# Optimization experiments

Measured on AMD Instinct MI355X. Metric: run time of the kernel, lower is better.

The kernel has to match this reference:

```python
import jax, jax.numpy as jnp
from jax import lax
import numpy as np

B, L, E, K, NCLS = 128, 1024, 8, 3, 5


def conv1d(x, w, b):
    # x: [N,C,L], w: [O,I,3], padding=1 -> same length
    y = lax.conv_general_dilated(x, w, (1,), [(1, 1)], dimension_numbers=('NCH', 'OIH', 'NCH'))
    return y + b[None, :, None]


def maxpool2(x):
    # MaxPool1d(kernel=2, stride=2), floor mode (VALID drops odd tail)
    return lax.reduce_window(x, -jnp.inf, lax.max, (1, 1, 2), (1, 1, 2), 'VALID')


def setup_inputs():
    key = jax.random.key(0)
    ks = jax.random.split(key, 32)
    s = 0.05
    g = lambda i, shp: jax.random.normal(ks[i], shp, jnp.float32) * s
    inp = {}
    inp['x'] = jax.random.normal(ks[0], (B, 1, L), jnp.float32)
    inp['c1_w'], inp['c1_b'] = g(1, (16, 1, 3)), jnp.zeros((16,), jnp.float32)
    # stacked expert conv params (leading dim = E)
    chans = [(16, 16), (16, 32), (32, 64), (64, 128), (128, 256), (256, 512)]
    for j, (ci, co) in enumerate(chans, start=1):
        inp[f'ew{j}'] = g(1 + j, (E, co, ci, 3))
        inp[f'eb{j}'] = jnp.zeros((E, co), jnp.float32)
    inp['r_w'], inp['r_b'] = g(10, (E, 16)), jnp.zeros((E,), jnp.float32)
    inp['c2_w'], inp['c2_b'] = g(11, (1024, 512, 3)), jnp.zeros((1024,), jnp.float32)
    fl = (L // 8 // 2) * 1024
    inp['f1_w'], inp['f1_b'] = g(12, (256, fl)) * 0.2, jnp.zeros((256,), jnp.float32)
    inp['f2_w'], inp['f2_b'] = g(13, (NCLS, 256)), jnp.zeros((NCLS,), jnp.float32)
    return inp


def reference(x, c1_w, c1_b, ew1, eb1, ew2, eb2, ew3, eb3, ew4, eb4, ew5, eb5, ew6, eb6,
              r_w, r_b, c2_w, c2_b, f1_w, f1_b, f2_w, f2_b):
    b = x.shape[0]
    h = jax.nn.relu(conv1d(x, c1_w, c1_b))            # [B,16,L]
    pooled = h.mean(axis=-1)                           # AdaptiveAvgPool1d(1) -> [B,16]
    # (router noise skipped: eval-mode determinism)
    rlogits = pooled @ r_w.T + r_b                     # [B,E]
    probs = jax.nn.softmax(rlogits, axis=-1)
    tg, ti = lax.top_k(probs, K)                       # [B,K]
    tg = tg / tg.sum(axis=-1, keepdims=True)
    gates = jnp.zeros((b, E), probs.dtype).at[jnp.arange(b)[:, None], ti].set(tg)  # dense [B,E]

    def expert(w1, b1, w2, b2, w3, b3, w4, b4, w5, b5, w6, b6):
        y = conv1d(h, w1, b1)
        y = maxpool2(jax.nn.relu(conv1d(y, w2, b2)))   # block1 -> [B,32,L/2]
        y = conv1d(y, w3, b3)
        y = maxpool2(jax.nn.relu(conv1d(y, w4, b4)))   # block2 -> [B,128,L/4]
        y = conv1d(y, w5, b5)
        y = maxpool2(jax.nn.relu(conv1d(y, w6, b6)))   # block3 -> [B,512,L/8]
        return y

    eouts = jax.vmap(expert)(ew1, eb1, ew2, eb2, ew3, eb3, ew4, eb4, ew5, eb5, ew6, eb6)  # [E,B,512,L/8]
    combined = jnp.einsum('be,ebcl->bcl', gates, eouts)  # gated scatter-combine (zero gate == not dispatched)

    y = maxpool2(jax.nn.relu(conv1d(combined, c2_w, c2_b)))  # [B,1024,L/16]
    y = y.reshape(b, -1)
    y = jax.nn.relu(y @ f1_w.T + f1_b)                 # dropout p=0.05 is identity in eval
    out = y @ f2_w.T + f2_b                            # [B,NCLS]

    mean_probs = probs.mean(axis=0)
    cv = jnp.std(mean_probs, ddof=1) / (mean_probs.mean() + 1e-10)  # torch std is unbiased
    return out, cv ** 2
```

## Files before the change

### kernel.cpp

```cpp
#include <hip/hip_runtime.h>
#include <hip/hip_bf16.h>
#include <math.h>

#define B_   128
#define L_   1024
#define E_   8
#define K_   3

typedef float f32x4 __attribute__((ext_vector_type(4)));
typedef short s8v  __attribute__((ext_vector_type(8)));
typedef unsigned short u16x8 __attribute__((ext_vector_type(8)));

__device__ inline ushort f2bf(float v) {
  union { float f; unsigned u; } x; x.f = v;
  unsigned r = (x.u + 0x7fffu + ((x.u >> 16) & 1u)) >> 16;
  return (ushort)r;
}
__device__ inline float bf2f(ushort h) {
  union { unsigned u; float f; } x; x.u = ((unsigned)h) << 16;
  return x.f;
}

__device__ __forceinline__ void gload_lds16(const ushort* g, ushort* l) {
  __builtin_amdgcn_global_load_lds(
      (const __attribute__((address_space(1))) unsigned int*)g,
      (__attribute__((address_space(3))) unsigned int*)l, 16, 0, 0);
}

__global__ __launch_bounds__(256) void conv1_k(
    const float* __restrict__ x, const float* __restrict__ w,
    const float* __restrict__ bias, float* __restrict__ h,
    float* __restrict__ pooled)
{
  const int b = blockIdx.x;
  const int t = threadIdx.x;
  __shared__ float xs[1026];
  __shared__ float wsm[48];
  __shared__ float bs[16];
  __shared__ float red[4][16];

  for (int i = t; i < 1024; i += 256) xs[i + 1] = x[(size_t)b * 1024 + i];
  if (t == 0) { xs[0] = 0.f; xs[1025] = 0.f; }
  if (t < 48) wsm[t] = w[t];
  if (t < 16) bs[t] = bias[t];
  __syncthreads();

  float ps[16];
#pragma unroll
  for (int c = 0; c < 16; ++c) ps[c] = 0.f;

  for (int li = 0; li < 4; ++li) {
    const int l = t + li * 256;
    const float xm = xs[l], x0 = xs[l + 1], xp = xs[l + 2];
#pragma unroll
    for (int co = 0; co < 16; ++co) {
      float v = fmaf(wsm[co * 3 + 0], xm,
                fmaf(wsm[co * 3 + 1], x0,
                fmaf(wsm[co * 3 + 2], xp, bs[co])));
      v = fmaxf(v, 0.f);
      h[((size_t)b * 16 + co) * 1024 + l] = v;
      ps[co] += v;
    }
  }
#pragma unroll
  for (int co = 0; co < 16; ++co) {
    float v = ps[co];
    for (int off = 32; off > 0; off >>= 1) v += __shfl_down(v, off, 64);
    ps[co] = v;
  }
  const int wid = t >> 6, lane = t & 63;
  if (lane == 0) {
#pragma unroll
    for (int co = 0; co < 16; ++co) red[wid][co] = ps[co];
  }
  __syncthreads();
  if (t < 16) pooled[(size_t)b * 16 + t] =
      (red[0][t] + red[1][t] + red[2][t] + red[3][t]) * (1.f / 1024.f);
}

__global__ void router_k(const float* __restrict__ pooled,
                         const float* __restrict__ rw,
                         const float* __restrict__ rb,
                         float* __restrict__ pair_g, int* __restrict__ pair_e,
                         float* __restrict__ cv2_out)
{
  const int b = threadIdx.x;
  __shared__ float pl[128][8];
  __shared__ float mp[8];

  float pv[16];
#pragma unroll
  for (int i = 0; i < 16; ++i) pv[i] = pooled[(size_t)b * 16 + i];

  float lg[8];
#pragma unroll
  for (int e = 0; e < 8; ++e) {
    float s = rb[e];
#pragma unroll
    for (int i = 0; i < 16; ++i) s = fmaf(pv[i], rw[e * 16 + i], s);
    lg[e] = s;
  }
  float mx = lg[0];
#pragma unroll
  for (int e = 1; e < 8; ++e) mx = fmaxf(mx, lg[e]);
  float pr[8]; float sum = 0.f;
#pragma unroll
  for (int e = 0; e < 8; ++e) { pr[e] = expf(lg[e] - mx); sum += pr[e]; }
  const float inv = 1.f / sum;
#pragma unroll
  for (int e = 0; e < 8; ++e) { pr[e] *= inv; pl[b][e] = pr[e]; }

  bool used[8] = {false,false,false,false,false,false,false,false};
  float tg[3]; int ti[3];
  for (int k = 0; k < 3; ++k) {
    float best = -1.f; int bi = 0;
#pragma unroll
    for (int e = 0; e < 8; ++e)
      if (!used[e] && pr[e] > best) { best = pr[e]; bi = e; }
    used[bi] = true; tg[k] = best; ti[k] = bi;
  }
  const float ts = 1.f / (tg[0] + tg[1] + tg[2]);
  for (int k = 0; k < 3; ++k) {
    pair_g[b * 3 + k] = tg[k] * ts;
    pair_e[b * 3 + k] = ti[k];
  }
  __syncthreads();
  if (b < 8) {
    float s = 0.f;
    for (int i = 0; i < 128; ++i) s += pl[i][b];
    mp[b] = s * (1.f / 128.f);
  }
  __syncthreads();
  if (b == 0) {
    float m = 0.f;
    for (int e = 0; e < 8; ++e) m += mp[e];
    m *= (1.f / 8.f);
    float v = 0.f;
    for (int e = 0; e < 8; ++e) { float d = mp[e] - m; v += d * d; }
    v *= (1.f / 7.f);
    const float cv = sqrtf(v) / (m + 1e-10f);
    cv2_out[0] = cv * cv;
  }
}

template <int CI, int CO, int LIN, bool POOL, int CIC, int CO_T, int CO_R,
          int IN_DIV>
__global__ __launch_bounds__(256) void convR_k(
    const float* __restrict__ in, const float* __restrict__ w,
    const float* __restrict__ bias, float* __restrict__ out,
    const int* __restrict__ pe)
{
  constexpr int CQ  = CO_T / CO_R;
  constexpr int LQ  = 256 / CQ;
  constexpr int L_T = LQ * 4;
  constexpr int LOUT = POOL ? (LIN / 2) : LIN;
  constexpr int RS  = L_T + 8;
  constexpr int CG  = CO_R / 4;

  const int p  = blockIdx.x;
  const int cb = blockIdx.y * CO_T;
  const int l0 = blockIdx.z * L_T;
  const int e  = pe ? pe[p] : 0;
  const float* inp = in + (size_t)(p / IN_DIV) * CI * LIN;
  const float* wp  = w + (size_t)e * CO * CI * 3;

  __shared__ float in_s[CIC * RS];
  __shared__ float w_s[CIC * 3 * CO_T];

  const int t  = threadIdx.x;
  const int cq = t / LQ;
  const int lq = t % LQ;

  float acc[CO_R][4];
#pragma unroll
  for (int c = 0; c < CO_R; ++c)
#pragma unroll
    for (int l = 0; l < 4; ++l) acc[c][l] = 0.f;

  for (int c0 = 0; c0 < CI; c0 += CIC) {
    for (int idx = t; idx < CIC * (L_T + 2); idx += 256) {
      const int ci = idx / (L_T + 2);
      const int j  = idx - ci * (L_T + 2);
      const int gl = l0 + j - 1;
      in_s[ci * RS + j] =
          (gl >= 0 && gl < LIN) ? inp[(size_t)(c0 + ci) * LIN + gl] : 0.f;
    }
    for (int i = t; i < CIC * CO_T; i += 256) {
      const int co = i % CO_T;
      const int ci = i / CO_T;
      const float* wsrc = wp + ((size_t)(cb + co) * CI + (c0 + ci)) * 3;
      const float w0 = wsrc[0], w1 = wsrc[1], w2 = wsrc[2];
      w_s[(ci * 3 + 0) * CO_T + co] = w0;
      w_s[(ci * 3 + 1) * CO_T + co] = w1;
      w_s[(ci * 3 + 2) * CO_T + co] = w2;
    }
    __syncthreads();
#pragma unroll 4
    for (int ci = 0; ci < CIC; ++ci) {
      const float* row = &in_s[ci * RS + lq * 4];
      const float4 xa = *reinterpret_cast<const float4*>(row);
      const float2 xb = *reinterpret_cast<const float2*>(row + 4);
      const float xv[6] = {xa.x, xa.y, xa.z, xa.w, xb.x, xb.y};
      const float* wrow = &w_s[ci * 3 * CO_T + cq * CO_R];
#pragma unroll
      for (int k = 0; k < 3; ++k) {
#pragma unroll
        for (int cg = 0; cg < CG; ++cg) {
          const float4 wv =
              *reinterpret_cast<const float4*>(&wrow[k * CO_T + cg * 4]);
          const float wq[4] = {wv.x, wv.y, wv.z, wv.w};
#pragma unroll
          for (int c = 0; c < 4; ++c)
#pragma unroll
            for (int l = 0; l < 4; ++l)
              acc[cg * 4 + c][l] = fmaf(wq[c], xv[l + k], acc[cg * 4 + c][l]);
        }
      }
    }
    __syncthreads();
  }

#pragma unroll
  for (int c = 0; c < CO_R; ++c) {
    const int co = cb + cq * CO_R + c;
    const float bv = bias[(size_t)e * CO + co];
    const float v0 = acc[c][0] + bv, v1 = acc[c][1] + bv;
    const float v2 = acc[c][2] + bv, v3 = acc[c][3] + bv;
    float* op = out + ((size_t)p * CO + co) * LOUT;
    if (POOL) {
      const int lo = (l0 >> 1) + lq * 2;
      float2 r;
      r.x = fmaxf(fmaxf(v0, v1), 0.f);
      r.y = fmaxf(fmaxf(v2, v3), 0.f);
      *reinterpret_cast<float2*>(&op[lo]) = r;
    } else {
      const int l = l0 + lq * 4;
      *reinterpret_cast<float4*>(&op[l]) = make_float4(v0, v1, v2, v3);
    }
  }
}

__global__ void wprep_k(const float* __restrict__ w, ushort* __restrict__ oh,
                        ushort* __restrict__ ol, int E, int CO, int CI,
                        int total)
{
  const int idx = blockIdx.x * 256 + threadIdx.x;
  if (idx >= total) return;
  const int KC = CI >> 5;
  const int j = idx & 31;
  int r = idx >> 5;
  const int co = r % CO; r /= CO;
  const int kc = r % KC; r /= KC;
  const int tp = r % 3;
  const int e  = r / 3;
  const float v = w[(((size_t)e * CO + co) * CI + (kc * 32 + j)) * 3 + tp];
  const ushort hi = f2bf(v);
  oh[idx] = hi;
  ol[idx] = f2bf(v - bf2f(hi));
}

__global__ __launch_bounds__(256) void t0_k(const float* __restrict__ in,
                                            ushort* __restrict__ oh,
                                            ushort* __restrict__ ol)
{
  __shared__ float tile[32][33];
  const int p  = blockIdx.x;
  const int l0 = blockIdx.y * 32;
  const int tx = threadIdx.x & 31;
  const int ty = threadIdx.x >> 5;

#pragma unroll
  for (int i = 0; i < 4; ++i) {
    const int ci = ty + i * 8;
    tile[ci][tx] = in[(size_t)p * 16384 + (size_t)ci * 512 + l0 + tx];
  }
  __syncthreads();
#pragma unroll
  for (int i = 0; i < 4; ++i) {
    const int l = l0 + ty + i * 8;
    const float v = tile[tx][ty + i * 8];
    const size_t o = ((size_t)p * 514 + 1 + l) * 32 + tx;
    const ushort hi = f2bf(v);
    oh[o] = hi;
    ol[o] = f2bf(v - bf2f(hi));
  }
  if (blockIdx.y == 0 && threadIdx.x < 32) {
    const size_t o0 = (size_t)p * 514 * 32 + threadIdx.x;
    const size_t o1 = ((size_t)p * 514 + 513) * 32 + threadIdx.x;
    oh[o0] = 0; ol[o0] = 0; oh[o1] = 0; ol[o1] = 0;
  }
}

__global__ __launch_bounds__(256) void t2_k(const float* __restrict__ comb,
                                            ushort* __restrict__ oh,
                                            ushort* __restrict__ ol)
{
  const size_t o4 = ((size_t)blockIdx.x * 256 + threadIdx.x) * 4;
  const int p = (int)(o4 / 66560);
  const int rem = (int)(o4 - (size_t)p * 66560);
  const int r = rem >> 9;
  const int c = rem & 511;
  ushort4 h4, l4;
  if (r == 0 || r == 129) {
    h4 = make_ushort4(0, 0, 0, 0);
    l4 = make_ushort4(0, 0, 0, 0);
  } else {
    const float4 v =
        *reinterpret_cast<const float4*>(&comb[((size_t)p * 128 + (r - 1)) * 512 + c]);
    h4.x = f2bf(v.x); l4.x = f2bf(v.x - bf2f(h4.x));
    h4.y = f2bf(v.y); l4.y = f2bf(v.y - bf2f(h4.y));
    h4.z = f2bf(v.z); l4.z = f2bf(v.z - bf2f(h4.z));
    h4.w = f2bf(v.w); l4.w = f2bf(v.w - bf2f(h4.w));
  }
  *reinterpret_cast<ushort4*>(&oh[o4]) = h4;
  *reinterpret_cast<ushort4*>(&ol[o4]) = l4;
}

template <int CI, int CO, int L, int OMODE>
__global__ __launch_bounds__(256) void convM_k(
    const ushort* __restrict__ xh, const ushort* __restrict__ xl,
    const ushort* __restrict__ wh, const ushort* __restrict__ wl,
    const float* __restrict__ bias,
    ushort* __restrict__ oh, ushort* __restrict__ ol,
    float* __restrict__ of,
    const int* __restrict__ pe, const float* __restrict__ pg,
    int pair0, int kpass)
{
  constexpr int KC = CI / 32;
  const int bx = blockIdx.x;
  const int cb = blockIdx.y * 64;
  const int lz = blockIdx.z * 128;

  int e = 0; float gate = 1.f;
  if (OMODE != 2) e = pe[pair0 + bx];
  if (OMODE == 1) gate = pg[pair0 + bx];
  const int lp = bx;

  __shared__ ushort xs[2][130][32];
  __shared__ ushort wsm[2][3][64][32];
  ushort* xsf = &xs[0][0][0];
  ushort* wsf = &wsm[0][0][0][0];

  const int t = threadIdx.x;
  const int lane = t & 63;
  const int wv = t >> 6;
  const int l16 = lane & 15;
  const int kb8 = (lane >> 4) * 8;

  f32x4 acc[2][4];
#pragma unroll
  for (int a = 0; a < 2; ++a)
#pragma unroll
    for (int b = 0; b < 4; ++b) acc[a][b] = (f32x4){0.f, 0.f, 0.f, 0.f};

  const size_t xbase = ((size_t)lp * (L + 2) + lz) * CI;

  for (int kc = 0; kc < KC; ++kc) {
    const int c0 = kc * 32;
#pragma unroll
    for (int it = 0; it < 5; ++it) {
      const int g = it * 256 + t;
      if (g < 1040) {
        const int pl = g >= 520;
        const int r = g - pl * 520;
        const int row = r >> 2;
        const int c16 = r & 3;
        const ushort* src =
            (pl ? xl : xh) + xbase + (size_t)row * CI + c0 + c16 * 8;
        gload_lds16(src, xsf + (size_t)g * 8);
      }
    }
#pragma unroll
    for (int it = 0; it < 6; ++it) {
      const int g = it * 256 + t;
      const int pl = g >= 768;
      const int r = g - pl * 768;
      const int tp = r >> 8;
      const int rr = r & 255;
      const int co = rr >> 2;
      const int c16 = rr & 3;
      const ushort* src = (pl ? wl : wh) +
          ((((size_t)e * 3 + tp) * KC + kc) * CO + cb + co) * 32 + c16 * 8;
      gload_lds16(src, wsf + (size_t)g * 8);
    }
    __syncthreads();

#pragma unroll
    for (int tp = 0; tp < 3; ++tp) {
      const int ar = wv * 32 + l16 + tp;
      s8v a00 = *reinterpret_cast<const s8v*>(&xs[0][ar][kb8]);
      s8v a01 = *reinterpret_cast<const s8v*>(&xs[0][ar + 16][kb8]);
      s8v a10 = *reinterpret_cast<const s8v*>(&xs[1][ar][kb8]);
      s8v a11 = *reinterpret_cast<const s8v*>(&xs[1][ar + 16][kb8]);
#pragma unroll
      for (int cs = 0; cs < 4; ++cs) {
        const int brow = cs * 16 + l16;
        s8v bh = *reinterpret_cast<const s8v*>(&wsm[0][tp][brow][kb8]);
        s8v bl = *reinterpret_cast<const s8v*>(&wsm[1][tp][brow][kb8]);
        acc[0][cs] = __builtin_amdgcn_mfma_f32_16x16x32_bf16(a00, bh, acc[0][cs], 0, 0, 0);
        acc[0][cs] = __builtin_amdgcn_mfma_f32_16x16x32_bf16(a00, bl, acc[0][cs], 0, 0, 0);
        acc[0][cs] = __builtin_amdgcn_mfma_f32_16x16x32_bf16(a10, bh, acc[0][cs], 0, 0, 0);
        acc[1][cs] = __builtin_amdgcn_mfma_f32_16x16x32_bf16(a01, bh, acc[1][cs], 0, 0, 0);
        acc[1][cs] = __builtin_amdgcn_mfma_f32_16x16x32_bf16(a01, bl, acc[1][cs], 0, 0, 0);
        acc[1][cs] = __builtin_amdgcn_mfma_f32_16x16x32_bf16(a11, bh, acc[1][cs], 0, 0, 0);
      }
    }
    __syncthreads();
  }

  float bv[4];
#pragma unroll
  for (int cs = 0; cs < 4; ++cs)
    bv[cs] = bias[(size_t)e * CO + cb + cs * 16 + l16];

  if (OMODE == 0) {
#pragma unroll
    for (int ls = 0; ls < 2; ++ls)
#pragma unroll
      for (int cs = 0; cs < 4; ++cs)
#pragma unroll
        for (int r = 0; r < 4; ++r) {
          const int l = lz + wv * 32 + ls * 16 + (lane >> 4) * 4 + r;
          const float v = acc[ls][cs][r] + bv[cs];
          const size_t o = ((size_t)lp * (L + 2) + 1 + l) * CO + cb + cs * 16 + l16;
          const ushort hi = f2bf(v);
          oh[o] = hi;
          ol[o] = f2bf(v - bf2f(hi));
        }
    if (blockIdx.z == 0 && t < 64) {
      const size_t o0 = (size_t)lp * (L + 2) * CO + cb + t;
      const size_t o1 = ((size_t)lp * (L + 2) + (L + 1)) * CO + cb + t;
      oh[o0] = 0; ol[o0] = 0; oh[o1] = 0; ol[o1] = 0;
    }
  } else if (OMODE == 3) {
#pragma unroll
    for (int ls = 0; ls < 2; ++ls)
#pragma unroll
      for (int cs = 0; cs < 4; ++cs)
#pragma unroll
        for (int r = 0; r < 4; r += 2) {
          const float v0 = acc[ls][cs][r] + bv[cs];
          const float v1 = acc[ls][cs][r + 1] + bv[cs];
          const float m = fmaxf(fmaxf(v0, v1), 0.f);
          const int lpp = (lz + wv * 32 + ls * 16 + (lane >> 4) * 4 + r) >> 1;
          const size_t o = ((size_t)lp * (L / 2 + 2) + 1 + lpp) * CO + cb + cs * 16 + l16;
          const ushort hi = f2bf(m);
          oh[o] = hi;
          ol[o] = f2bf(m - bf2f(hi));
        }
    if (blockIdx.z == 0 && t < 64) {
      const size_t o0 = (size_t)lp * (L / 2 + 2) * CO + cb + t;
      const size_t o1 = ((size_t)lp * (L / 2 + 2) + (L / 2 + 1)) * CO + cb + t;
      oh[o0] = 0; ol[o0] = 0; oh[o1] = 0; ol[o1] = 0;
    }
  } else if (OMODE == 1) {
#pragma unroll
    for (int ls = 0; ls < 2; ++ls)
#pragma unroll
      for (int cs = 0; cs < 4; ++cs)
#pragma unroll
        for (int r = 0; r < 4; r += 2) {
          const float v0 = acc[ls][cs][r] + bv[cs];
          const float v1 = acc[ls][cs][r + 1] + bv[cs];
          const float m = fmaxf(fmaxf(v0, v1), 0.f);
          const int lpp = (lz + wv * 32 + ls * 16 + (lane >> 4) * 4 + r) >> 1;
          const int co = cb + cs * 16 + l16;
          of[((size_t)bx * (L / 2) + lpp) * CO + co] = gate * m;
        }
  } else {
#pragma unroll
    for (int ls = 0; ls < 2; ++ls)
#pragma unroll
      for (int cs = 0; cs < 4; ++cs)
#pragma unroll
        for (int r = 0; r < 4; r += 2) {
          const float v0 = acc[ls][cs][r] + bv[cs];
          const float v1 = acc[ls][cs][r + 1] + bv[cs];
          const float m = fmaxf(fmaxf(v0, v1), 0.f);
          const int lpp = (lz + wv * 32 + ls * 16 + (lane >> 4) * 4 + r) >> 1;
          const int co = cb + cs * 16 + l16;
          const size_t o = ((size_t)lp * CO + co) * (L / 2) + lpp;
          of[o] = m;
        }
  }
}

__global__ void combine3_k(const float4* __restrict__ y6,
                           float4* __restrict__ outc, int total4)
{
  const int idx = blockIdx.x * 256 + threadIdx.x;
  if (idx >= total4) return;
  const int b = idx >> 14;
  const int r = idx & 16383;
  const float4 a = y6[(size_t)(b * 3 + 0) * 16384 + r];
  const float4 c = y6[(size_t)(b * 3 + 1) * 16384 + r];
  const float4 d = y6[(size_t)(b * 3 + 2) * 16384 + r];
  float4 o;
  o.x = a.x + c.x + d.x;
  o.y = a.y + c.y + d.y;
  o.z = a.z + c.z + d.z;
  o.w = a.w + c.w + d.w;
  outc[idx] = o;
}

__global__ __launch_bounds__(256) void fc1M_k(const float* __restrict__ X,
                                              const float* __restrict__ W,
                                              float* __restrict__ part)
{
  __shared__ ushort xs[2][128][32];
  __shared__ ushort wsm[2][64][32];
  const int t = threadIdx.x;
  const int lane = t & 63;
  const int wv = t >> 6;
  const int l16 = lane & 15;
  const int kb8 = (lane >> 4) * 8;
  const int ot = blockIdx.x * 64;
  const size_t k0g = (size_t)blockIdx.y * 512;

  f32x4 acc[2][4];
#pragma unroll
  for (int a = 0; a < 2; ++a)
#pragma unroll
    for (int b = 0; b < 4; ++b) acc[a][b] = (f32x4){0.f, 0.f, 0.f, 0.f};

  const int xrow = t >> 1;
  const int xcol = (t & 1) * 16;
  const int wco  = t >> 2;
  const int wk   = (t & 3) * 8;

  for (int it = 0; it < 16; ++it) {
    const size_t k0 = k0g + it * 32;
    {
      const float* src = X + (size_t)xrow * 65536 + k0 + xcol;
      float v[16];
#pragma unroll
      for (int q = 0; q < 4; ++q)
        *reinterpret_cast<float4*>(&v[q * 4]) =
            *reinterpret_cast<const float4*>(src + q * 4);
#pragma unroll
      for (int q = 0; q < 2; ++q) {
        u16x8 hv, lv;
#pragma unroll
        for (int j = 0; j < 8; ++j) {
          const float f = v[q * 8 + j];
          const ushort h = f2bf(f);
          hv[j] = h;
          lv[j] = f2bf(f - bf2f(h));
        }
        *reinterpret_cast<u16x8*>(&xs[0][xrow][xcol + q * 8]) = hv;
        *reinterpret_cast<u16x8*>(&xs[1][xrow][xcol + q * 8]) = lv;
      }
    }
    {
      const float* src = W + (size_t)(ot + wco) * 65536 + k0 + wk;
      float v[8];
      *reinterpret_cast<float4*>(&v[0]) = *reinterpret_cast<const float4*>(src);
      *reinterpret_cast<float4*>(&v[4]) = *reinterpret_cast<const float4*>(src + 4);
      u16x8 hv, lv;
#pragma unroll
      for (int j = 0; j < 8; ++j) {
        const ushort h = f2bf(v[j]);
        hv[j] = h;
        lv[j] = f2bf(v[j] - bf2f(h));
      }
      *reinterpret_cast<u16x8*>(&wsm[0][wco][wk]) = hv;
      *reinterpret_cast<u16x8*>(&wsm[1][wco][wk]) = lv;
    }
    __syncthreads();
#pragma unroll
    for (int ms = 0; ms < 2; ++ms) {
      const int ar = wv * 32 + ms * 16 + l16;
      s8v ah = *reinterpret_cast<const s8v*>(&xs[0][ar][kb8]);
      s8v al = *reinterpret_cast<const s8v*>(&xs[1][ar][kb8]);
#pragma unroll
      for (int cs = 0; cs < 4; ++cs) {
        const int brow = cs * 16 + l16;
        s8v bh = *reinterpret_cast<const s8v*>(&wsm[0][brow][kb8]);
        s8v bl = *reinterpret_cast<const s8v*>(&wsm[1][brow][kb8]);
        acc[ms][cs] = __builtin_amdgcn_mfma_f32_16x16x32_bf16(ah, bh, acc[ms][cs], 0, 0, 0);
        acc[ms][cs] = __builtin_amdgcn_mfma_f32_16x16x32_bf16(ah, bl, acc[ms][cs], 0, 0, 0);
        acc[ms][cs] = __builtin_amdgcn_mfma_f32_16x16x32_bf16(al, bh, acc[ms][cs], 0, 0, 0);
      }
    }
    __syncthreads();
  }

#pragma unroll
  for (int ms = 0; ms < 2; ++ms)
#pragma unroll
    for (int cs = 0; cs < 4; ++cs)
#pragma unroll
      for (int r = 0; r < 4; ++r) {
        const int row = wv * 32 + ms * 16 + (lane >> 4) * 4 + r;
        const int col = ot + cs * 16 + l16;
        part[((size_t)blockIdx.y * 128 + row) * 256 + col] = acc[ms][cs][r];
      }
}

__global__ void fc1red_k(const float* __restrict__ part,
                         const float* __restrict__ b1, float* __restrict__ o1)
{
  const int idx = blockIdx.x * 256 + threadIdx.x;
  if (idx < 32768) {
    float s = 0.f;
#pragma unroll 8
    for (int z = 0; z < 128; ++z) s += part[(size_t)z * 32768 + idx];
    o1[idx] = fmaxf(s + b1[idx & 255], 0.f);
  }
}

__global__ void fc2_k(const float* __restrict__ o1, const float* __restrict__ w2,
                      const float* __restrict__ b2, float* __restrict__ out)
{
  const int b = blockIdx.x;
  const int lane = threadIdx.x;
  float acc[5] = {0.f, 0.f, 0.f, 0.f, 0.f};
  for (int i = lane; i < 256; i += 64) {
    const float xv = o1[(size_t)b * 256 + i];
#pragma unroll
    for (int o = 0; o < 5; ++o) acc[o] = fmaf(xv, w2[o * 256 + i], acc[o]);
  }
#pragma unroll
  for (int o = 0; o < 5; ++o) {
    for (int off = 32; off > 0; off >>= 1)
      acc[o] += __shfl_down(acc[o], off, 64);
  }
  if (lane == 0) {
#pragma unroll
    for (int o = 0; o < 5; ++o) out[b * 5 + o] = acc[o] + b2[o];
  }
}

extern "C" void kernel_launch(void* const* d_in, const int* in_sizes, int n_in,
                              void* d_out, int out_size, void* d_ws,
                              size_t ws_size, hipStream_t stream)
{
  const float* x   = (const float*)d_in[0];
  const float* c1w = (const float*)d_in[1];
  const float* c1b = (const float*)d_in[2];
  const float* ew[6];
  const float* eb[6];
  for (int j = 0; j < 6; ++j) {
    ew[j] = (const float*)d_in[3 + 2 * j];
    eb[j] = (const float*)d_in[4 + 2 * j];
  }
  const float* rw  = (const float*)d_in[15];
  const float* rb  = (const float*)d_in[16];
  const float* c2w = (const float*)d_in[17];
  const float* c2b = (const float*)d_in[18];
  const float* f1w = (const float*)d_in[19];
  const float* f1b = (const float*)d_in[20];
  const float* f2w = (const float*)d_in[21];
  const float* f2b = (const float*)d_in[22];
  float* out = (float*)d_out;

  const int chunkB = (ws_size >= 170000000ull) ? 32 : 16;
  const int chunkP = chunkB * 3;
  const int nchunk = 128 / chunkB;

  char* basep = (char*)d_ws;
  size_t off = 0;
  auto alloc = [&](size_t bytes) -> void* {
    off = (off + 255) & ~(size_t)255;
    void* r = basep + off;
    off += bytes;
    return r;
  };

  float* h      = (float*)alloc(2097152ull * 4);
  float* pooled = (float*)alloc(2048ull * 4);
  float* pairg  = (float*)alloc(384ull * 4);
  int*   paire  = (int*)  alloc(384ull * 4);
  float* fc1o   = (float*)alloc(32768ull * 4);
  float* comb   = (float*)alloc(8388608ull * 4);
  const size_t chunk_base = (off + 255) & ~(size_t)255;
  float*  bufA  = (float*)alloc((size_t)chunkP * 16384 * 4);
  float*  bufB  = (float*)alloc((size_t)chunkP * 16384 * 4);
  ushort* xt3h  = (ushort*)alloc((size_t)chunkP * 16448 * 2);
  ushort* xt3l  = (ushort*)alloc((size_t)chunkP * 16448 * 2);
  ushort* yE3h  = (ushort*)alloc((size_t)chunkP * 32896 * 2);
  ushort* yE3l  = (ushort*)alloc((size_t)chunkP * 32896 * 2);
  ushort* xt5h  = (ushort*)alloc((size_t)chunkP * 33024 * 2);
  ushort* xt5l  = (ushort*)alloc((size_t)chunkP * 33024 * 2);
  ushort* y5h   = (ushort*)alloc((size_t)chunkP * 66048 * 2);
  ushort* y5l   = (ushort*)alloc((size_t)chunkP * 66048 * 2);
  float*  y6    = (float*)alloc((size_t)chunkP * 65536 * 4);
  ushort* xtFh  = (ushort*)(basep + chunk_base);
  ushort* xtFl  = xtFh + 8519680ull;
  float* part   = (float*)(basep + chunk_base);
  ushort* wp3h  = (ushort*)alloc(49152ull * 2);
  ushort* wp3l  = (ushort*)alloc(49152ull * 2);
  ushort* wp4h  = (ushort*)alloc(196608ull * 2);
  ushort* wp4l  = (ushort*)alloc(196608ull * 2);
  ushort* wp5h  = (ushort*)alloc(786432ull * 2);
  ushort* wp5l  = (ushort*)alloc(786432ull * 2);
  ushort* wp6h  = (ushort*)alloc(3145728ull * 2);
  ushort* wp6l  = (ushort*)alloc(3145728ull * 2);
  ushort* wpFh  = (ushort*)alloc(1572864ull * 2);
  ushort* wpFl  = (ushort*)alloc(1572864ull * 2);

  conv1_k<<<128, 256, 0, stream>>>(x, c1w, c1b, h, pooled);
  router_k<<<1, 128, 0, stream>>>(pooled, rw, rb, pairg, paire, out + 640);

  wprep_k<<<(49152 + 255) / 256, 256, 0, stream>>>(ew[2], wp3h, wp3l, 8, 64, 32, 49152);
  wprep_k<<<(196608 + 255) / 256, 256, 0, stream>>>(ew[3], wp4h, wp4l, 8, 128, 64, 196608);
  wprep_k<<<(786432 + 255) / 256, 256, 0, stream>>>(ew[4], wp5h, wp5l, 8, 256, 128, 786432);
  wprep_k<<<(3145728 + 255) / 256, 256, 0, stream>>>(ew[5], wp6h, wp6l, 8, 512, 256, 3145728);
  wprep_k<<<(1572864 + 255) / 256, 256, 0, stream>>>(c2w, wpFh, wpFl, 1, 1024, 512, 1572864);

  for (int c = 0; c < nchunk; ++c) {
    const int b0 = c * chunkB;
    const int p0 = c * chunkP;
    convR_k<16, 16, 1024, false, 16, 16, 4, 3>
        <<<dim3(chunkP, 1, 4), 256, 0, stream>>>(
            h + (size_t)b0 * 16 * 1024, ew[0], eb[0], bufA, paire + p0);
    convR_k<16, 32, 1024, true, 16, 32, 8, 1>
        <<<dim3(chunkP, 1, 4), 256, 0, stream>>>(bufA, ew[1], eb[1], bufB,
                                                 paire + p0);
    t0_k<<<dim3(chunkP, 16), 256, 0, stream>>>(bufB, xt3h, xt3l);
    convM_k<32, 64, 512, 0>
        <<<dim3(chunkP, 1, 4), 256, 0, stream>>>(xt3h, xt3l, wp3h, wp3l, eb[2],
                                                 yE3h, yE3l, nullptr, paire,
                                                 nullptr, p0, 0);
    convM_k<64, 128, 512, 3>
        <<<dim3(chunkP, 2, 4), 256, 0, stream>>>(yE3h, yE3l, wp4h, wp4l, eb[3],
                                                 xt5h, xt5l, nullptr, paire,
                                                 nullptr, p0, 0);
    convM_k<128, 256, 256, 0>
        <<<dim3(chunkP, 4, 2), 256, 0, stream>>>(xt5h, xt5l, wp5h, wp5l, eb[4],
                                                 y5h, y5l, nullptr, paire,
                                                 nullptr, p0, 0);
    convM_k<256, 512, 256, 1>
        <<<dim3(chunkP, 8, 2), 256, 0, stream>>>(y5h, y5l, wp6h, wp6l, eb[5],
                                                 nullptr, nullptr, y6,
                                                 paire, pairg, p0, 0);
    combine3_k<<<(chunkB * 16384 + 255) / 256, 256, 0, stream>>>(
        (const float4*)y6, (float4*)(comb + (size_t)b0 * 65536),
        chunkB * 16384);
  }

  t2_k<<<8320, 256, 0, stream>>>(comb, xtFh, xtFl);
  convM_k<512, 1024, 128, 2>
      <<<dim3(128, 16, 1), 256, 0, stream>>>(xtFh, xtFl, wpFh, wpFl, c2b,
                                             nullptr, nullptr, comb, nullptr,
                                             nullptr, 0, 0);

  fc1M_k<<<dim3(4, 128), 256, 0, stream>>>(comb, f1w, part);
  fc1red_k<<<128, 256, 0, stream>>>(part, f1b, fc1o);
  fc2_k<<<128, 64, 0, stream>>>(fc1o, f2w, f2b, out);
}
```

Before: 684.3 us.

## Add 32x32x16 MFMA conv kernel with 128-wide channel tiles for late layers

```diff
diff --git a/kernel.cpp b/kernel.cpp
--- a/kernel.cpp
+++ b/kernel.cpp
@@ -7,8 +7,9 @@
 #define E_   8
 #define K_   3
 
-typedef float f32x4 __attribute__((ext_vector_type(4)));
-typedef short s8v  __attribute__((ext_vector_type(8)));
+typedef float f32x4  __attribute__((ext_vector_type(4)));
+typedef float f32x16 __attribute__((ext_vector_type(16)));
+typedef short s8v    __attribute__((ext_vector_type(8)));
 typedef unsigned short u16x8 __attribute__((ext_vector_type(8)));
 
 __device__ inline ushort f2bf(float v) {
@@ -482,6 +483,198 @@
           const size_t o = ((size_t)lp * CO + co) * (L / 2) + lpp;
           of[o] = m;
         }
+  }
+}
+
+template <int CI, int CO, int L, int OMODE>
+__global__ __launch_bounds__(256) void convM32_k(
+    const ushort* __restrict__ xh, const ushort* __restrict__ xl,
+    const ushort* __restrict__ wh, const ushort* __restrict__ wl,
+    const float* __restrict__ bias,
+    ushort* __restrict__ oh, ushort* __restrict__ ol,
+    float* __restrict__ of,
+    const int* __restrict__ pe, const float* __restrict__ pg, int pair0)
+{
+  constexpr int KC = CI / 32;
+  const int bx = blockIdx.x;
+  const int cb = blockIdx.y * 128;
+  const int lz = blockIdx.z * 128;
+
+  int e = 0; float gate = 1.f;
+  if (OMODE != 2) e = pe[pair0 + bx];
+  if (OMODE == 1) gate = pg[pair0 + bx];
+  const int lp = bx;
+
+  __shared__ ushort xs[2][130][32];
+  __shared__ ushort wsm[2][3][128][32];
+  ushort* xsf = &xs[0][0][0];
+  ushort* wsf = &wsm[0][0][0][0];
+
+  const int t = threadIdx.x;
+  const int lane = t & 63;
+  const int wv = t >> 6;
+  const int wlb = (wv >> 1) * 64;
+  const int wcb = (wv & 1) * 64;
+  const int l31 = lane & 31;
+  const int khi = lane >> 5;
+
+  f32x16 acc[2][2];
+#pragma unroll
+  for (int a = 0; a < 2; ++a)
+#pragma unroll
+    for (int b = 0; b < 2; ++b)
+#pragma unroll
+      for (int q = 0; q < 16; ++q) acc[a][b][q] = 0.f;
+
+  const size_t xbase = ((size_t)lp * (L + 2) + lz) * CI;
+
+  for (int kc = 0; kc < KC; ++kc) {
+    const int c0 = kc * 32;
+#pragma unroll
+    for (int it = 0; it < 5; ++it) {
+      const int g = it * 256 + t;
+      if (g < 1040) {
+        const int pl = g >= 520;
+        const int r = g - pl * 520;
+        const int row = r >> 2;
+        const int c16 = (r & 3) ^ ((row >> 1) & 3);
+        const ushort* src =
+            (pl ? xl : xh) + xbase + (size_t)row * CI + c0 + c16 * 8;
+        gload_lds16(src, xsf + (size_t)g * 8);
+      }
+    }
+#pragma unroll
+    for (int it = 0; it < 12; ++it) {
+      const int g = it * 256 + t;
+      const int pl = g >= 1536;
+      const int r = g - pl * 1536;
+      const int tp = r >> 9;
+      const int rr = r & 511;
+      const int co = rr >> 2;
+      const int c16 = (rr & 3) ^ ((co >> 1) & 3);
+      const ushort* src = (pl ? wl : wh) +
+          ((((size_t)e * 3 + tp) * KC + kc) * CO + cb + co) * 32 + c16 * 8;
+      gload_lds16(src, wsf + (size_t)g * 8);
+    }
+    __syncthreads();
+
+#pragma unroll
+    for (int tp = 0; tp < 3; ++tp) {
+#pragma unroll
+      for (int kh = 0; kh < 2; ++kh) {
+        s8v av[2][2];
+#pragma unroll
+        for (int lt = 0; lt < 2; ++lt) {
+          const int row = wlb + lt * 32 + l31 + tp;
+          const int gsw = ((kh * 2 + khi) ^ ((row >> 1) & 3)) * 8;
+          av[0][lt] = *reinterpret_cast<const s8v*>(&xs[0][row][gsw]);
+          av[1][lt] = *reinterpret_cast<const s8v*>(&xs[1][row][gsw]);
+        }
+#pragma unroll
+        for (int ct = 0; ct < 2; ++ct) {
+          const int wrow = wcb + ct * 32 + l31;
+          const int gsw = ((kh * 2 + khi) ^ ((wrow >> 1) & 3)) * 8;
+          s8v bh_ = *reinterpret_cast<const s8v*>(&wsm[0][tp][wrow][gsw]);
+          s8v bl_ = *reinterpret_cast<const s8v*>(&wsm[1][tp][wrow][gsw]);
+#pragma unroll
+          for (int lt = 0; lt < 2; ++lt) {
+            acc[lt][ct] = __builtin_amdgcn_mfma_f32_32x32x16_bf16(
+                av[0][lt], bh_, acc[lt][ct], 0, 0, 0);
+            acc[lt][ct] = __builtin_amdgcn_mfma_f32_32x32x16_bf16(
+                av[0][lt], bl_, acc[lt][ct], 0, 0, 0);
+            acc[lt][ct] = __builtin_amdgcn_mfma_f32_32x32x16_bf16(
+                av[1][lt], bh_, acc[lt][ct], 0, 0, 0);
+          }
+        }
+      }
+    }
+    __syncthreads();
+  }
+
+  float bv2[2];
+#pragma unroll
+  for (int ct = 0; ct < 2; ++ct)
+    bv2[ct] = bias[(size_t)e * CO + cb + wcb + ct * 32 + l31];
+
+  if (OMODE == 0) {
+#pragma unroll
+    for (int lt = 0; lt < 2; ++lt)
+#pragma unroll
+      for (int ct = 0; ct < 2; ++ct) {
+        const int co = cb + wcb + ct * 32 + l31;
+#pragma unroll
+        for (int reg = 0; reg < 16; ++reg) {
+          const int row = (reg & 3) + 8 * (reg >> 2) + 4 * khi;
+          const int l = lz + wlb + lt * 32 + row;
+          const float v = acc[lt][ct][reg] + bv2[ct];
+          const size_t o = ((size_t)lp * (L + 2) + 1 + l) * CO + co;
+          const ushort hi = f2bf(v);
+          oh[o] = hi;
+          ol[o] = f2bf(v - bf2f(hi));
+        }
+      }
+    if (blockIdx.z == 0 && t < 128) {
+      const size_t o0 = (size_t)lp * (L + 2) * CO + cb + t;
+      const size_t o1 = ((size_t)lp * (L + 2) + (L + 1)) * CO + cb + t;
+      oh[o0] = 0; ol[o0] = 0; oh[o1] = 0; ol[o1] = 0;
+    }
+  } else if (OMODE == 3) {
+#pragma unroll
+    for (int lt = 0; lt < 2; ++lt)
+#pragma unroll
+      for (int ct = 0; ct < 2; ++ct) {
+        const int co = cb + wcb + ct * 32 + l31;
+#pragma unroll
+        for (int reg = 0; reg < 16; reg += 2) {
+          const int row = (reg & 3) + 8 * (reg >> 2) + 4 * khi;
+          const float v0 = acc[lt][ct][reg] + bv2[ct];
+          const float v1 = acc[lt][ct][reg + 1] + bv2[ct];
+          const float m = fmaxf(fmaxf(v0, v1), 0.f);
+          const int lpp = (lz + wlb + lt * 32 + row) >> 1;
+          const size_t o = ((size_t)lp * (L / 2 + 2) + 1 + lpp) * CO + co;
+          const ushort hi = f2bf(m);
+          oh[o] = hi;
+          ol[o] = f2bf(m - bf2f(hi));
+        }
+      }
+    if (blockIdx.z == 0 && t < 128) {
+      const size_t o0 = (size_t)lp * (L / 2 + 2) * CO + cb + t;
+      const size_t o1 = ((size_t)lp * (L / 2 + 2) + (L / 2 + 1)) * CO + cb + t;
+      oh[o0] = 0; ol[o0] = 0; oh[o1] = 0; ol[o1] = 0;
+    }
+  } else if (OMODE == 1) {
+#pragma unroll
+    for (int lt = 0; lt < 2; ++lt)
+#pragma unroll
+      for (int ct = 0; ct < 2; ++ct) {
+        const int co = cb + wcb + ct * 32 + l31;
+#pragma unroll
+        for (int reg = 0; reg < 16; reg += 2) {
+          const int row = (reg & 3) + 8 * (reg >> 2) + 4 * khi;
+          const float v0 = acc[lt][ct][reg] + bv2[ct];
+          const float v1 = acc[lt][ct][reg + 1] + bv2[ct];
+          const float m = fmaxf(fmaxf(v0, v1), 0.f);
+          const int lpp = (lz + wlb + lt * 32 + row) >> 1;
+          of[((size_t)bx * (L / 2) + lpp) * CO + co] = gate * m;
+        }
+      }
+  } else {
+#pragma unroll
+    for (int lt = 0; lt < 2; ++lt)
+#pragma unroll
+      for (int ct = 0; ct < 2; ++ct) {
+        const int co = cb + wcb + ct * 32 + l31;
+#pragma unroll
+        for (int reg = 0; reg < 16; reg += 2) {
+          const int row = (reg & 3) + 8 * (reg >> 2) + 4 * khi;
+          const float v0 = acc[lt][ct][reg] + bv2[ct];
+          const float v1 = acc[lt][ct][reg + 1] + bv2[ct];
+          const float m = fmaxf(fmaxf(v0, v1), 0.f);
+          const int lpp = (lz + wlb + lt * 32 + row) >> 1;
+          const size_t o = ((size_t)lp * CO + co) * (L / 2) + lpp;
+          of[o] = m;
+        }
+      }
   }
 }
 
@@ -722,28 +915,28 @@
         <<<dim3(chunkP, 1, 4), 256, 0, stream>>>(xt3h, xt3l, wp3h, wp3l, eb[2],
                                                  yE3h, yE3l, nullptr, paire,
                                                  nullptr, p0, 0);
-    convM_k<64, 128, 512, 3>
-        <<<dim3(chunkP, 2, 4), 256, 0, stream>>>(yE3h, yE3l, wp4h, wp4l, eb[3],
+    convM32_k<64, 128, 512, 3>
+        <<<dim3(chunkP, 1, 4), 256, 0, stream>>>(yE3h, yE3l, wp4h, wp4l, eb[3],
                                                  xt5h, xt5l, nullptr, paire,
-                                                 nullptr, p0, 0);
-    convM_k<128, 256, 256, 0>
-        <<<dim3(chunkP, 4, 2), 256, 0, stream>>>(xt5h, xt5l, wp5h, wp5l, eb[4],
+                                                 nullptr, p0);
+    convM32_k<128, 256, 256, 0>
+        <<<dim3(chunkP, 2, 2), 256, 0, stream>>>(xt5h, xt5l, wp5h, wp5l, eb[4],
                                                  y5h, y5l, nullptr, paire,
-                                                 nullptr, p0, 0);
-    convM_k<256, 512, 256, 1>
-        <<<dim3(chunkP, 8, 2), 256, 0, stream>>>(y5h, y5l, wp6h, wp6l, eb[5],
+                                                 nullptr, p0);
+    convM32_k<256, 512, 256, 1>
+        <<<dim3(chunkP, 4, 2), 256, 0, stream>>>(y5h, y5l, wp6h, wp6l, eb[5],
                                                  nullptr, nullptr, y6,
-                                                 paire, pairg, p0, 0);
+                                                 paire, pairg, p0);
     combine3_k<<<(chunkB * 16384 + 255) / 256, 256, 0, stream>>>(
         (const float4*)y6, (float4*)(comb + (size_t)b0 * 65536),
         chunkB * 16384);
   }
 
   t2_k<<<8320, 256, 0, stream>>>(comb, xtFh, xtFl);
-  convM_k<512, 1024, 128, 2>
-      <<<dim3(128, 16, 1), 256, 0, stream>>>(xtFh, xtFl, wpFh, wpFl, c2b,
-                                             nullptr, nullptr, comb, nullptr,
-                                             nullptr, 0, 0);
+  convM32_k<512, 1024, 128, 2>
+      <<<dim3(128, 8, 1), 256, 0, stream>>>(xtFh, xtFl, wpFh, wpFl, c2b,
+                                            nullptr, nullptr, comb, nullptr,
+                                            nullptr, 0);
 
   fc1M_k<<<dim3(4, 128), 256, 0, stream>>>(comb, f1w, part);
   fc1red_k<<<128, 256, 0, stream>>>(part, f1b, fc1o);
```

Measured after the change: 756.5 us. 10.6% more time.
